# Kernel tuning notes

Hardware: AMD Instinct MI355X
Metric: run time of the kernel (lower is better)

Reference implementation:

```python
import jax, jax.numpy as jnp
import numpy as np

MAX_ITER = 20
TOL = 1e-8
N = 4096


def setup_inputs() -> dict:
    key = jax.random.key(0)
    kA, kb = jax.random.split(key)
    R = jax.random.normal(kA, (N, N), dtype=jnp.float32)
    # SPD conditioning so CG is well-posed (solver assumes an SPD-ish system)
    A = R @ R.T / jnp.float32(N) + jnp.eye(N, dtype=jnp.float32)
    b = jax.random.normal(kb, (N,), dtype=jnp.float32)
    return {"A": A, "b": b}


def _cg(A, b):
    # identity preconditioner: M = I, so M_A = A, M_b = b
    xk = jnp.zeros_like(b)
    rk = b - A @ xk
    pk = rk

    def cond(state):
        k, xk, rk, pk = state
        return jnp.logical_and(k < MAX_ITER, jnp.linalg.norm(rk) >= TOL)

    def body(state):
        k, xk, rk, pk = state
        Apk = A @ pk                      # [N] matvec, the memory-bound core op
        rk_dot = rk @ rk
        ak = rk_dot / (pk @ Apk)
        xk1 = xk + ak * pk
        rk1 = rk - ak * Apk
        bk = (rk1 @ rk1) / rk_dot
        pk1 = rk1 + bk * pk
        return (k + 1, xk1, rk1, pk1)

    _, xk, _, _ = jax.lax.while_loop(cond, body, (jnp.int32(0), xk, rk, pk))
    return xk


def reference(A, b):
    return _cg(A, b)
```

## Files before the change

### kernel.cpp

```cpp
#include <hip/hip_runtime.h>

#define CGN    4096
#define NBLK   256
#define NTHR   1024
#define NW     (NTHR / 64)
#define RPB    (CGN / NBLK)
#define MAX_IT 20
#define TOLF   1e-8f

typedef float f32x4 __attribute__((ext_vector_type(4)));

__device__ float    g_Ap[2][CGN];
__device__ unsigned g_flags[NBLK];
__device__ unsigned g_release;

#define AL(p)   __hip_atomic_load((p), __ATOMIC_RELAXED, __HIP_MEMORY_SCOPE_AGENT)
#define AS(p,v) __hip_atomic_store((p), (v), __ATOMIC_RELAXED, __HIP_MEMORY_SCOPE_AGENT)

__device__ __forceinline__ float wave_reduce(float v) {
    #pragma unroll
    for (int off = 32; off > 0; off >>= 1)
        v += __shfl_down(v, off, 64);
    return v;
}

__device__ __forceinline__ void grid_barrier(int blk, int tid, unsigned target) {
    __syncthreads();
    if (tid == 0) AS(&g_flags[blk], target);
    if (blk == 0) {
        if (tid < NBLK) {
            while ((int)(AL(&g_flags[tid]) - target) < 0)
                __builtin_amdgcn_s_sleep(2);
        }
        __syncthreads();
        if (tid == 0) AS(&g_release, target);
    } else {
        if (tid == 0) {
            while ((int)(AL(&g_release) - target) < 0)
                __builtin_amdgcn_s_sleep(2);
        }
    }
    __syncthreads();
}

__device__ __forceinline__ void block_sum3(float a, float b, float c,
                                           float* red, int lane, int wv,
                                           float* oa, float* ob, float* oc) {
    a = wave_reduce(a);
    b = wave_reduce(b);
    c = wave_reduce(c);
    __syncthreads();
    if (lane == 0) {
        red[wv]          = a;
        red[NW + wv]     = b;
        red[2 * NW + wv] = c;
    }
    __syncthreads();
    float ta = 0.f, tb = 0.f, tc = 0.f;
    #pragma unroll
    for (int i = 0; i < NW; ++i) {
        ta += red[i];
        tb += red[NW + i];
        tc += red[2 * NW + i];
    }
    *oa = ta; *ob = tb; *oc = tc;
}

__global__ __launch_bounds__(NTHR, 4) void pcg_kernel(
    const float* __restrict__ A, const float* __restrict__ b,
    float* __restrict__ x)
{
    __shared__ float p_lds[CGN];
    __shared__ float red[3 * NW];

    const int tid  = threadIdx.x;
    const int blk  = blockIdx.x;
    const int lane = tid & 63;
    const int wv   = tid >> 6;
    const int e0   = tid * 4;
    const bool owner = (tid >> 2) == blk;

    const unsigned base = AL(&g_flags[blk]);
    unsigned bc = 0;

    f32x4 arow[16];
    {
        const f32x4* bp = (const f32x4*)(A + (size_t)(blk * RPB + wv) * CGN) + lane;
        #pragma unroll
        for (int j = 0; j < 16; ++j) {
            const f32x4* addr = bp + j * 64;
            asm volatile("global_load_dwordx4 %0, %1, off"
                         : "=v"(arow[j]) : "v"(addr));
        }
    }

    f32x4 r_reg = ((const f32x4*)b)[tid];
    f32x4 p_reg = r_reg;
    f32x4 x_reg = {0.f, 0.f, 0.f, 0.f};
    *(f32x4*)&p_lds[e0] = p_reg;
    float rs, d1, d2;
    block_sum3(r_reg[0]*r_reg[0] + r_reg[1]*r_reg[1]
             + r_reg[2]*r_reg[2] + r_reg[3]*r_reg[3], 0.f, 0.f,
               red, lane, wv, &rs, &d1, &d2);

    asm volatile("s_waitcnt vmcnt(0)" ::: "memory");
    __builtin_amdgcn_sched_barrier(0);

    for (int k = 0; k < MAX_IT; ++k) {
        if (!(rs >= TOLF * TOLF)) break;
        const int buf = k & 1;

        float acc = 0.f;
        #pragma unroll
        for (int j = 0; j < 16; ++j) {
            f32x4 p4 = *(const f32x4*)&p_lds[(j * 64 + lane) * 4];
            acc += arow[j][0] * p4[0] + arow[j][1] * p4[1]
                 + arow[j][2] * p4[2] + arow[j][3] * p4[3];
        }
        acc = wave_reduce(acc);
        if (lane == 0) AS(&g_Ap[buf][blk * RPB + wv], acc);

        grid_barrier(blk, tid, base + (++bc));

        f32x4 ap4;
        #pragma unroll
        for (int i = 0; i < 4; ++i) ap4[i] = AL(&g_Ap[buf][e0 + i]);

        float pAp, rAp, ApAp;
        block_sum3(p_reg[0]*ap4[0] + p_reg[1]*ap4[1]
                 + p_reg[2]*ap4[2] + p_reg[3]*ap4[3],
                   r_reg[0]*ap4[0] + r_reg[1]*ap4[1]
                 + r_reg[2]*ap4[2] + r_reg[3]*ap4[3],
                   ap4[0]*ap4[0] + ap4[1]*ap4[1]
                 + ap4[2]*ap4[2] + ap4[3]*ap4[3],
                   red, lane, wv, &pAp, &rAp, &ApAp);

        float ak = rs / pAp;
        float rs_new = rs - 2.f * ak * rAp + ak * ak * ApAp;
        float bk = rs_new / rs;
        rs = rs_new;

        if (owner) {
            #pragma unroll
            for (int i = 0; i < 4; ++i) x_reg[i] += ak * p_reg[i];
        }
        #pragma unroll
        for (int i = 0; i < 4; ++i) {
            r_reg[i] -= ak * ap4[i];
            p_reg[i]  = r_reg[i] + bk * p_reg[i];
        }
        *(f32x4*)&p_lds[e0] = p_reg;
        __syncthreads();
    }

    if (owner) *(f32x4*)&x[e0] = x_reg;
}

extern "C" void kernel_launch(void* const* d_in, const int* in_sizes, int n_in,
                              void* d_out, int out_size, void* d_ws, size_t ws_size,
                              hipStream_t stream) {
    const float* A = (const float*)d_in[0];
    const float* b = (const float*)d_in[1];
    float* x = (float*)d_out;
    pcg_kernel<<<dim3(NBLK), dim3(NTHR), 0, stream>>>(A, b, x);
}
```

Measured before the change: 80.00 us.

## Replace centralized grid barrier with epoch-tagged per-element dataflow polling

Removes the two-level flag/release grid barrier. Each wave's Ap result is now packed into a 64-bit word together with an iteration epoch tag, and consumers spin on exactly the elements they need until the tag matches. This is meant to cut barrier latency and the serialized release hop through block 0. The trade-off is that every thread polls global memory on four entries, which raises L2 traffic. A per-block epoch counter is kept across launches so the tags stay consistent.

```diff
diff --git a/kernel.cpp b/kernel.cpp
--- a/kernel.cpp
+++ b/kernel.cpp
@@ -9,38 +9,21 @@
 #define TOLF   1e-8f
 
 typedef float f32x4 __attribute__((ext_vector_type(4)));
+typedef unsigned long long u64;
 
-__device__ float    g_Ap[2][CGN];
-__device__ unsigned g_flags[NBLK];
-__device__ unsigned g_release;
+__device__ u64      g_ap[2][CGN];
+__device__ unsigned g_epoch[NBLK];
 
-#define AL(p)   __hip_atomic_load((p), __ATOMIC_RELAXED, __HIP_MEMORY_SCOPE_AGENT)
-#define AS(p,v) __hip_atomic_store((p), (v), __ATOMIC_RELAXED, __HIP_MEMORY_SCOPE_AGENT)
+#define AL32(p)   __hip_atomic_load((p), __ATOMIC_RELAXED, __HIP_MEMORY_SCOPE_AGENT)
+#define AS32(p,v) __hip_atomic_store((p), (v), __ATOMIC_RELAXED, __HIP_MEMORY_SCOPE_AGENT)
+#define AL64(p)   __hip_atomic_load((p), __ATOMIC_RELAXED, __HIP_MEMORY_SCOPE_AGENT)
+#define AS64(p,v) __hip_atomic_store((p), (v), __ATOMIC_RELAXED, __HIP_MEMORY_SCOPE_AGENT)
 
 __device__ __forceinline__ float wave_reduce(float v) {
     #pragma unroll
     for (int off = 32; off > 0; off >>= 1)
         v += __shfl_down(v, off, 64);
     return v;
-}
-
-__device__ __forceinline__ void grid_barrier(int blk, int tid, unsigned target) {
-    __syncthreads();
-    if (tid == 0) AS(&g_flags[blk], target);
-    if (blk == 0) {
-        if (tid < NBLK) {
-            while ((int)(AL(&g_flags[tid]) - target) < 0)
-                __builtin_amdgcn_s_sleep(2);
-        }
-        __syncthreads();
-        if (tid == 0) AS(&g_release, target);
-    } else {
-        if (tid == 0) {
-            while ((int)(AL(&g_release) - target) < 0)
-                __builtin_amdgcn_s_sleep(2);
-        }
-    }
-    __syncthreads();
 }
 
 __device__ __forceinline__ void block_sum3(float a, float b, float c,
@@ -80,8 +63,7 @@
     const int e0   = tid * 4;
     const bool owner = (tid >> 2) == blk;
 
-    const unsigned base = AL(&g_flags[blk]);
-    unsigned bc = 0;
+    const unsigned base = AL32(&g_epoch[blk]);
 
     f32x4 arow[16];
     {
@@ -106,9 +88,11 @@
     asm volatile("s_waitcnt vmcnt(0)" ::: "memory");
     __builtin_amdgcn_sched_barrier(0);
 
+    unsigned kdone = 0;
     for (int k = 0; k < MAX_IT; ++k) {
         if (!(rs >= TOLF * TOLF)) break;
         const int buf = k & 1;
+        const unsigned tgt = base + (unsigned)k + 1u;
 
         float acc = 0.f;
         #pragma unroll
@@ -118,13 +102,23 @@
                  + arow[j][2] * p4[2] + arow[j][3] * p4[3];
         }
         acc = wave_reduce(acc);
-        if (lane == 0) AS(&g_Ap[buf][blk * RPB + wv], acc);
-
-        grid_barrier(blk, tid, base + (++bc));
+        if (lane == 0) {
+            u64 w = ((u64)tgt << 32) | (u64)(unsigned)__float_as_uint(acc);
+            AS64(&g_ap[buf][blk * RPB + wv], w);
+        }
+        asm volatile("s_waitcnt vmcnt(0)" ::: "memory");
+        __builtin_amdgcn_sched_barrier(0);
 
         f32x4 ap4;
         #pragma unroll
-        for (int i = 0; i < 4; ++i) ap4[i] = AL(&g_Ap[buf][e0 + i]);
+        for (int i = 0; i < 4; ++i) {
+            u64 w = AL64(&g_ap[buf][e0 + i]);
+            while ((int)((unsigned)(w >> 32) - tgt) < 0) {
+                __builtin_amdgcn_s_sleep(4);
+                w = AL64(&g_ap[buf][e0 + i]);
+            }
+            ap4[i] = __uint_as_float((unsigned)w);
+        }
 
         float pAp, rAp, ApAp;
         block_sum3(p_reg[0]*ap4[0] + p_reg[1]*ap4[1]
@@ -151,7 +145,10 @@
         }
         *(f32x4*)&p_lds[e0] = p_reg;
         __syncthreads();
+        kdone = (unsigned)k + 1u;
     }
+
+    if (tid == 0) AS32(&g_epoch[blk], base + kdone);
 
     if (owner) *(f32x4*)&x[e0] = x_reg;
 }
```

Result: slower. 83.08 us (+3.9%).
